# Optimization experiments

Hardware: AMD Instinct MI355X
Metric: run time of the kernel (lower is better)

The kernel has to match this reference:

```python
import jax, jax.numpy as jnp
import numpy as np

B, N, M, NS = 4, 32768, 1024, 32
RADIUS = 0.1
EPS = 1e-5
CHANS = [16, 32, 32, 64]


def setup_inputs() -> dict:
    key = jax.random.key(0)
    ks = jax.random.split(key, 8)
    d = {
        'theta': jax.random.uniform(ks[0], (B, N), jnp.float32, 0.0, float(np.pi)),
        'phi': jax.random.uniform(ks[1], (B, N), jnp.float32, 0.0, 2.0 * float(np.pi)),
        'features': jax.random.normal(ks[2], (B, CHANS[0], N), jnp.float32),
    }
    for i, (ci, co) in enumerate(zip(CHANS[:-1], CHANS[1:])):
        d[f'w{i}'] = jax.random.normal(jax.random.fold_in(ks[3], i), (co, ci), jnp.float32) * 0.1
        d[f'b{i}'] = jnp.zeros((co,), jnp.float32)
        d[f'g{i}'] = jnp.ones((co,), jnp.float32)
        d[f'be{i}'] = jnp.zeros((co,), jnp.float32)
    return d


def _group(theta, phi, features):
    # angular ball query + random neighbor sampling (deterministic key),
    # duplicates padded with the first valid neighbor (max-pool invariant,
    # matching the torch code's sampling-with-replacement semantics).
    k1, k2 = jax.random.split(jax.random.key(42))
    n = theta.shape[1]
    cent_idx = jax.random.permutation(k1, n)[:M]                 # shared across batch, like torch code
    ct = theta[:, cent_idx]                                      # (B, M)
    cp = phi[:, cent_idx]
    th_s, ph_s = jax.lax.stop_gradient(theta), jax.lax.stop_gradient(phi)
    ct_s, cp_s = jax.lax.stop_gradient(ct), jax.lax.stop_gradient(cp)
    dist = jnp.sqrt((th_s[:, None, :] - ct_s[:, :, None]) ** 2 +
                    (ph_s[:, None, :] - cp_s[:, :, None]) ** 2)  # (B, M, N)
    mask = dist <= RADIUS
    scores = jnp.where(mask, jax.random.uniform(k2, dist.shape, jnp.float32), jnp.inf)
    _, idx = jax.lax.top_k(-scores, NS)                          # NS random in-ball indices, (B, M, NS)
    valid = jnp.take_along_axis(mask, idx, axis=-1)
    idx = jnp.where(valid, idx, idx[..., :1])                    # centroid itself is always valid at slot 0
    gathered = jax.vmap(lambda f, i: f[:, i])(features, idx)     # (B, C, M, NS)
    grouped = jnp.transpose(gathered, (0, 1, 3, 2))              # (B, C, NS, M)
    return ct, cp, grouped


def _mlp_max(x, params):
    # 1x1 conv + BatchNorm (batch stats, training mode) + ReLU stack, then max over nsample
    for w, b, g, be in params:
        x = jnp.einsum('oc,bcsm->bosm', w, x) + b[None, :, None, None]
        mu = x.mean(axis=(0, 2, 3), keepdims=True)
        var = x.var(axis=(0, 2, 3), keepdims=True)
        x = (x - mu) * jax.lax.rsqrt(var + EPS) * g[None, :, None, None] + be[None, :, None, None]
        x = jax.nn.relu(x)
    return x.max(axis=2)                                         # (B, C_out, M)


def reference(theta, phi, features, w0, b0, g0, be0, w1, b1, g1, be1, w2, b2, g2, be2):
    params = [(w0, b0, g0, be0), (w1, b1, g1, be1), (w2, b2, g2, be2)]
    ct, cp, grouped = _group(theta, phi, features)
    new_feats = _mlp_max(grouped, params)
    return ct, cp, new_feats
```

## Files before the change

kernel.cpp:

```cpp
#include <hip/hip_runtime.h>
#include <stdint.h>

#define N_PTS 32768
#define M_CENT 1024
#define B_SZ 4
#define NS 32
#define NR 64
#define P_TOT (B_SZ * NS * M_CENT)

#define GT 29
#define GP 58
#define NCELL (GT * GP)
#define INVF (1.0f / 0.11f)
#define CAPW 320

__device__ __forceinline__ int cell_t(float t) {
  return min(GT - 1, (int)(t * INVF));
}
__device__ __forceinline__ int cell_p(float p) {
  return min(GP - 1, (int)(p * INVF));
}

struct Key2 { uint32_t a, b; };

__device__ __forceinline__ uint32_t rotl32(uint32_t v, uint32_t r) {
  return (v << r) | (v >> (32u - r));
}

__device__ __forceinline__ void tf2x32(uint32_t k0, uint32_t k1,
                                       uint32_t& x0, uint32_t& x1) {
  uint32_t ks0 = k0, ks1 = k1, ks2 = k0 ^ k1 ^ 0x1BD11BDAu;
  x0 += ks0; x1 += ks1;
#define TF_ROUND(r) { x0 += x1; x1 = rotl32(x1, r); x1 ^= x0; }
  TF_ROUND(13u) TF_ROUND(15u) TF_ROUND(26u) TF_ROUND(6u)
  x0 += ks1; x1 += ks2 + 1u;
  TF_ROUND(17u) TF_ROUND(29u) TF_ROUND(16u) TF_ROUND(24u)
  x0 += ks2; x1 += ks0 + 2u;
  TF_ROUND(13u) TF_ROUND(15u) TF_ROUND(26u) TF_ROUND(6u)
  x0 += ks0; x1 += ks1 + 3u;
  TF_ROUND(17u) TF_ROUND(29u) TF_ROUND(16u) TF_ROUND(24u)
  x0 += ks1; x1 += ks2 + 4u;
  TF_ROUND(13u) TF_ROUND(15u) TF_ROUND(26u) TF_ROUND(6u)
  x0 += ks2; x1 += ks0 + 5u;
#undef TF_ROUND
}

__device__ __forceinline__ Key2 tf_block(Key2 k, uint32_t hi, uint32_t lo) {
  uint32_t x0 = hi, x1 = lo;
  tf2x32(k.a, k.b, x0, x1);
  Key2 r; r.a = x0; r.b = x1; return r;
}

__global__ __launch_bounds__(256) void prep_kernel(const float* __restrict__ theta,
                                                   const float* __restrict__ phi,
                                                   uint32_t* __restrict__ bits1,
                                                   uint32_t* __restrict__ bits2,
                                                   int* __restrict__ hist1,
                                                   int* __restrict__ hist2,
                                                   int* __restrict__ cellcnt) {
  int j = blockIdx.x * 256 + threadIdx.x;
  int b = j >> 15;
  float t = theta[j], p = phi[j];
  atomicAdd(&cellcnt[b * NCELL + cell_t(t) * GP + cell_p(p)], 1);
  if (j < N_PTS) {
    Key2 root; root.a = 0u; root.b = 42u;
    Key2 k1   = tf_block(root, 0u, 0u);
    Key2 keyA = tf_block(k1, 0u, 0u);
    Key2 sub1 = tf_block(k1, 0u, 1u);
    Key2 sub2 = tf_block(keyA, 0u, 1u);
    Key2 r1 = tf_block(sub1, 0u, (uint32_t)j);
    Key2 r2 = tf_block(sub2, 0u, (uint32_t)j);
    uint32_t v1 = r1.a ^ r1.b, v2 = r2.a ^ r2.b;
    bits1[j] = v1; bits2[j] = v2;
    atomicAdd(&hist1[v1 >> 16], 1);
    atomicAdd(&hist2[v2 >> 16], 1);
  }
}

__global__ __launch_bounds__(256) void transpose_kernel(const float* __restrict__ feat,
                                                        float* __restrict__ featT) {
  __shared__ float lds[16][65];
  int b = blockIdx.y;
  int n0 = blockIdx.x * 64;
  int tid = threadIdx.x;
#pragma unroll
  for (int k = 0; k < 4; ++k) {
    int v = tid + k * 256;
    int c = v >> 6, no = v & 63;
    lds[c][no] = feat[((size_t)(b * 16 + c) << 15) + n0 + no];
  }
  __syncthreads();
#pragma unroll
  for (int k = 0; k < 4; ++k) {
    int v = tid + k * 256;
    int no = v >> 4, c = v & 15;
    featT[((size_t)(b << 15) + n0 + no) * 16 + c] = lds[c][no];
  }
}

__global__ __launch_bounds__(256) void scans_kernel(const int* __restrict__ hist1,
                                                    const int* __restrict__ hist2,
                                                    int* __restrict__ gbase1,
                                                    int* __restrict__ gbase2,
                                                    const int* __restrict__ cellcnt,
                                                    int* __restrict__ cellpre,
                                                    int* __restrict__ cellcur) {
  __shared__ int s[256];
  int t = threadIdx.x;
  if (blockIdx.x < 2) {
    const int* hist = blockIdx.x == 0 ? hist1 : hist2;
    int* gbase = blockIdx.x == 0 ? gbase1 : gbase2;
    int sum = 0;
    for (int i = 0; i < 256; ++i) sum += hist[t * 256 + i];
    s[t] = sum;
    __syncthreads();
    if (t == 0) {
      int run = 0;
      for (int i = 0; i < 256; ++i) { int v = s[i]; s[i] = run; run += v; }
    }
    __syncthreads();
    gbase[t] = s[t];
  } else {
    int b = blockIdx.x - 2;
    const int* cnt = cellcnt + b * NCELL;
    int i0 = t * 7, i1 = min(i0 + 7, NCELL);
    int sum = 0;
    for (int i = i0; i < i1; ++i) sum += cnt[i];
    s[t] = sum;
    __syncthreads();
    for (int off = 1; off < 256; off <<= 1) {
      int v = (t >= off) ? s[t - off] : 0;
      __syncthreads();
      s[t] += v;
      __syncthreads();
    }
    int run = (t == 0) ? 0 : s[t - 1];
    for (int i = i0; i < i1; ++i) {
      cellpre[b * NCELL + i] = run;
      cellcur[b * NCELL + i] = run;
      run += cnt[i];
    }
  }
}

__global__ __launch_bounds__(256) void bucket_scan_kernel(const int* __restrict__ hist1,
                                                          const int* __restrict__ hist2,
                                                          const int* __restrict__ gbase1,
                                                          const int* __restrict__ gbase2,
                                                          int* __restrict__ prefix1,
                                                          int* __restrict__ prefix2,
                                                          int* __restrict__ cursor1,
                                                          int* __restrict__ cursor2) {
  __shared__ int s[256];
  const int* hist = blockIdx.y == 0 ? hist1 : hist2;
  const int* gbase = blockIdx.y == 0 ? gbase1 : gbase2;
  int* prefix = blockIdx.y == 0 ? prefix1 : prefix2;
  int* cursor = blockIdx.y == 0 ? cursor1 : cursor2;
  int g = blockIdx.x, t = threadIdx.x;
  int idx = g * 256 + t;
  int orig = hist[idx];
  s[t] = orig;
  __syncthreads();
  for (int off = 1; off < 256; off <<= 1) {
    int v = (t >= off) ? s[t - off] : 0;
    __syncthreads();
    s[t] += v;
    __syncthreads();
  }
  int pref = gbase[g] + s[t] - orig;
  prefix[idx] = pref;
  cursor[idx] = pref;
}

__global__ __launch_bounds__(256) void scatter_kernel(const float* __restrict__ theta,
                                                      const float* __restrict__ phi,
                                                      int* __restrict__ cellcur,
                                                      float4* __restrict__ pts4,
                                                      const uint32_t* __restrict__ bits1,
                                                      const uint32_t* __restrict__ bits2,
                                                      int* __restrict__ cursor1,
                                                      int* __restrict__ cursor2,
                                                      int* __restrict__ sorted1,
                                                      int* __restrict__ sorted2) {
  int j = blockIdx.x * 256 + threadIdx.x;
  int b = j >> 15, n = j & (N_PTS - 1);
  float t = theta[j], p = phi[j];
  int cell = b * NCELL + cell_t(t) * GP + cell_p(p);
  int pos = atomicAdd(&cellcur[cell], 1);
  pts4[(b << 15) + pos] = make_float4(t, p, __int_as_float(n), 0.0f);
  if (j < N_PTS) {
    int p1 = atomicAdd(&cursor1[bits1[j] >> 16], 1);
    sorted1[p1] = j;
    int p2 = atomicAdd(&cursor2[bits2[j] >> 16], 1);
    sorted2[p2] = j;
  }
}

__device__ __forceinline__ int exact_rank(const uint32_t* __restrict__ bits,
                                          const int* __restrict__ prefix,
                                          const int* __restrict__ hist,
                                          const int* __restrict__ sorted, int j) {
  uint32_t my = bits[j];
  int b = (int)(my >> 16);
  int start = prefix[b];
  int cnt = hist[b];
  int r = start;
  for (int i = 0; i < cnt; ++i) {
    int m = sorted[start + i];
    uint32_t vb = bits[m];
    if (vb < my || (vb == my && m < j)) ++r;
  }
  return r;
}

__global__ __launch_bounds__(256) void rank_scatter1_kernel(
    const uint32_t* __restrict__ bits1, const uint32_t* __restrict__ bits2,
    const int* __restrict__ prefix1, const int* __restrict__ prefix2,
    const int* __restrict__ hist1, const int* __restrict__ hist2,
    const int* __restrict__ sorted1, const int* __restrict__ sorted2,
    int* __restrict__ xmid, int* __restrict__ rank2) {
  int j = blockIdx.x * 256 + threadIdx.x;
  int r1 = exact_rank(bits1, prefix1, hist1, sorted1, j);
  xmid[r1] = j;
  rank2[j] = exact_rank(bits2, prefix2, hist2, sorted2, j);
}

__global__ __launch_bounds__(256) void scatter2_kernel(const int* __restrict__ rank2,
                                                       const int* __restrict__ xmid,
                                                       int* __restrict__ xfin) {
  int p = blockIdx.x * 256 + threadIdx.x;
  xfin[rank2[p]] = xmid[p];
}

__global__ __launch_bounds__(256) void select_kernel(
    const float* __restrict__ theta, const float* __restrict__ phi,
    const int* __restrict__ cent,
    const int* __restrict__ cellpre, const int* __restrict__ cellcnt,
    const float4* __restrict__ pts4,
    int* __restrict__ idx_buf, float* __restrict__ out_ct, float* __restrict__ out_cp) {
  __shared__ float wsc[4][CAPW];
  __shared__ int wsn[4][CAPW];
  int tid = threadIdx.x;
  int w = tid >> 6, lane = tid & 63;
  int bm = blockIdx.x * 4 + w;
  int b = bm >> 10, m = bm & 1023;
  int ci = cent[m];
  float ctv = theta[(b << 15) + ci];
  float cpv = phi[(b << 15) + ci];
  if (lane == 0) { out_ct[bm] = ctv; out_cp[bm] = cpv; }

  Key2 root; root.a = 0u; root.b = 42u;
  Key2 k2 = tf_block(root, 0u, 1u);
  uint32_t flat_base = (uint32_t)bm << 15;

  int tc = cell_t(ctv), pc = cell_p(cpv);
  int t0 = max(0, tc - 1), t1 = min(GT - 1, tc + 1);
  int p0 = max(0, pc - 1), p1 = min(GP - 1, pc + 1);
  int nct = t1 - t0 + 1, ncp = p1 - p0 + 1, ncells = nct * ncp;

  int cst = 0, ccn = 0;
  if (lane < ncells) {
    int cell = b * NCELL + (t0 + lane / ncp) * GP + (p0 + lane % ncp);
    cst = cellpre[cell];
    ccn = cellcnt[cell];
  }
  int sc9[9], cc9[9];
#pragma unroll
  for (int k = 0; k < 9; ++k) {
    sc9[k] = __shfl(cst, k);
    cc9[k] = __shfl(ccn, k);
  }
  int T = 0;
#pragma unroll
  for (int k = 0; k < 9; ++k) T += cc9[k];

  const float4* bpts = pts4 + ((size_t)b << 15);
  int wcnt = 0;
  for (int base = 0; base < T; base += 64) {
    int i = base + lane;
    bool hit = false; float sc = 0.0f; int n = 0;
    if (i < T) {
      int gidx = 0, acc = 0;
#pragma unroll
      for (int k = 0; k < 9; ++k) {
        int lo = acc; acc += cc9[k];
        if (i >= lo && i < acc) gidx = sc9[k] + (i - lo);
      }
      float4 pt = bpts[gidx];
      float dx = __fsub_rn(pt.x, ctv);
      float dy = __fsub_rn(pt.y, cpv);
      float d = __fsqrt_rn(__fadd_rn(__fmul_rn(dx, dx), __fmul_rn(dy, dy)));
      if (d <= 0.1f) {
        hit = true; n = __float_as_int(pt.z);
        Key2 r = tf_block(k2, 0u, flat_base + (uint32_t)n);
        uint32_t bits = r.a ^ r.b;
        sc = __uint_as_float(0x3f800000u | (bits >> 9)) - 1.0f;
      }
    }
    unsigned long long mask = __ballot(hit);
    int pos = wcnt + __popcll(mask & ((1ull << lane) - 1ull));
    if (hit && pos < CAPW) { wsc[w][pos] = sc; wsn[w][pos] = n; }
    wcnt = min(wcnt + (int)__popcll(mask), CAPW);
  }

  int mysel;
  if (wcnt <= 64) {
    float s = (lane < wcnt) ? wsc[w][lane] : 3.0e38f;
    int n = (lane < wcnt) ? wsn[w][lane] : 0x7fffffff;
#pragma unroll
    for (int k = 2; k <= 64; k <<= 1) {
#pragma unroll
      for (int jj = k >> 1; jj > 0; jj >>= 1) {
        float os = __shfl_xor(s, jj);
        int on = __shfl_xor(n, jj);
        bool lower = (lane & jj) == 0;
        bool dir = (lane & k) == 0;
        bool mineFirst = (s < os) || (s == os && n < on);
        bool takeMine = ((lower == mineFirst) == dir);
        s = takeMine ? s : os;
        n = takeMine ? n : on;
      }
    }
    int n0 = __shfl(n, 0);
    mysel = (lane < wcnt) ? n : n0;
  } else {
    float ls = -1.0f; int ln = -1;
    int sel0 = -1; mysel = -1;
    for (int r = 0; r < NS; ++r) {
      float best = 3.0e38f; int bn = 0x7fffffff;
      for (int i = lane; i < wcnt; i += 64) {
        float s = wsc[w][i]; int n = wsn[w][i];
        bool after = (s > ls) || (s == ls && n > ln);
        bool better = (s < best) || (s == best && n < bn);
        if (after && better) { best = s; bn = n; }
      }
      for (int off = 32; off; off >>= 1) {
        float os = __shfl_xor(best, off);
        int on = __shfl_xor(bn, off);
        if (os < best || (os == best && on < bn)) { best = os; bn = on; }
      }
      int chosen;
      if (best < 3.0e38f) { ls = best; ln = bn; chosen = bn; }
      else chosen = sel0;
      if (r == 0) sel0 = chosen;
      if (lane == r) mysel = chosen;
    }
  }
  if (lane < NS) idx_buf[bm * NS + lane] = mysel;
}

__device__ __forceinline__ float bn_relu(float y, float mu, float r, float g, float be) {
  float t = __fsub_rn(y, mu);
  t = __fmul_rn(t, r);
  t = __fmul_rn(t, g);
  t = __fadd_rn(t, be);
  return fmaxf(t, 0.0f);
}

template <int CO>
__device__ __forceinline__ void accum_stats_pad(const float* __restrict__ Yp,
                                                double* __restrict__ S, int tid, int bid) {
  if (tid < CO) {
    double s1 = 0.0, s2 = 0.0;
#pragma unroll
    for (int s = 0; s < NS; ++s) {
      double v = (double)Yp[tid * 33 + s];
      s1 += v; s2 += v * v;
    }
    double* base = S + (size_t)(bid & (NR - 1)) * (2 * CO);
    atomicAdd(base + tid, s1);
    atomicAdd(base + CO + tid, s2);
  }
}

__global__ __launch_bounds__(256) void pass1_kernel(
    const float* __restrict__ feat, const float* __restrict__ featT,
    const int* __restrict__ idx_buf,
    const float* __restrict__ w0, const float* __restrict__ b0,
    float* __restrict__ stash, double* __restrict__ stats, int mode) {
  __shared__ int idxs[NS];
  __shared__ float X1[512];
  __shared__ float Yp[32 * 33];
  int bm = blockIdx.x, tid = threadIdx.x, b = bm >> 10;
  if (tid < NS) idxs[tid] = idx_buf[bm * NS + tid];
  __syncthreads();
  if (mode == 3) {
    if (tid < 128) {
      int s = tid >> 2, c4 = tid & 3;
      float4 f = *reinterpret_cast<const float4*>(
          &featT[((size_t)(b << 15) + idxs[s]) * 16 + c4 * 4]);
      X1[(c4 * 4 + 0) * 32 + s] = f.x;
      X1[(c4 * 4 + 1) * 32 + s] = f.y;
      X1[(c4 * 4 + 2) * 32 + s] = f.z;
      X1[(c4 * 4 + 3) * 32 + s] = f.w;
    }
  } else {
    for (int v = tid; v < 512; v += 256) {
      int c = v >> 5, s = v & 31;
      float val = feat[(size_t)(b * 16 + c) * N_PTS + idxs[s]];
      X1[v] = val;
      if (mode == 1) stash[(size_t)bm * 512 + v] = val;
    }
  }
  __syncthreads();
  for (int v = tid; v < 1024; v += 256) {
    int o = v >> 5, s = v & 31;
    float acc = b0[o];
#pragma unroll
    for (int c = 0; c < 16; ++c) acc = fmaf(w0[o * 16 + c], X1[c * 32 + s], acc);
    Yp[o * 33 + s] = acc;
    if (mode >= 2) stash[(size_t)bm * 1024 + v] = acc;
  }
  __syncthreads();
  accum_stats_pad<32>(Yp, stats, tid, bm);
}

__global__ __launch_bounds__(256) void pass2s_kernel(
    const float* __restrict__ Y1g,
    const float* __restrict__ mur1, const float* __restrict__ g0, const float* __restrict__ be0,
    const float* __restrict__ w1, const float* __restrict__ b1,
    double* __restrict__ stats) {
  __shared__ float X2[1024];
  __shared__ float Yp[32 * 33];
  int bm = blockIdx.x, tid = threadIdx.x;
  for (int v = tid; v < 1024; v += 256) {
    int o = v >> 5;
    X2[v] = bn_relu(Y1g[(size_t)bm * 1024 + v], mur1[o], mur1[32 + o], g0[o], be0[o]);
  }
  __syncthreads();
  for (int v = tid; v < 1024; v += 256) {
    int o = v >> 5, s = v & 31;
    float acc = b1[o];
#pragma unroll
    for (int c = 0; c < 32; ++c) acc = fmaf(w1[o * 32 + c], X2[c * 32 + s], acc);
    Yp[o * 33 + s] = acc;
  }
  __syncthreads();
  accum_stats_pad<32>(Yp, stats, tid, bm);
}

__global__ __launch_bounds__(256) void pass3s_kernel(
    const float* __restrict__ Y1g,
    const float* __restrict__ mur1, const float* __restrict__ g0, const float* __restrict__ be0,
    const float* __restrict__ w1, const float* __restrict__ b1,
    const float* __restrict__ mur2, const float* __restrict__ g1, const float* __restrict__ be1,
    const float* __restrict__ w2, const float* __restrict__ b2,
    float* __restrict__ mm3, double* __restrict__ stats) {
  __shared__ float X2[1024];
  __shared__ float X3[1024];
  __shared__ float Yp[64 * 33];
  int bm = blockIdx.x, tid = threadIdx.x;
  for (int v = tid; v < 1024; v += 256) {
    int o = v >> 5;
    X2[v] = bn_relu(Y1g[(size_t)bm * 1024 + v], mur1[o], mur1[32 + o], g0[o], be0[o]);
  }
  __syncthreads();
  for (int v = tid; v < 1024; v += 256) {
    int o = v >> 5, s = v & 31;
    float acc = b1[o];
#pragma unroll
    for (int c = 0; c < 32; ++c) acc = fmaf(w1[o * 32 + c], X2[c * 32 + s], acc);
    X3[v] = bn_relu(acc, mur2[o], mur2[32 + o], g1[o], be1[o]);
  }
  __syncthreads();
  for (int v = tid; v < 2048; v += 256) {
    int o = v >> 5, s = v & 31;
    float acc = b2[o];
#pragma unroll
    for (int c = 0; c < 32; ++c) acc = fmaf(w2[o * 32 + c], X3[c * 32 + s], acc);
    Yp[o * 33 + s] = acc;
  }
  __syncthreads();
  if (tid < 64) {
    double s1 = 0.0, s2 = 0.0;
    float mx = -3.0e38f, mn = 3.0e38f;
#pragma unroll
    for (int s = 0; s < NS; ++s) {
      float y = Yp[tid * 33 + s];
      double v = (double)y;
      s1 += v; s2 += v * v;
      mx = fmaxf(mx, y); mn = fminf(mn, y);
    }
    double* base = stats + (size_t)(bm & (NR - 1)) * 128;
    atomicAdd(base + tid, s1);
    atomicAdd(base + 64 + tid, s2);
    mm3[bm * 128 + tid * 2] = mx;
    mm3[bm * 128 + tid * 2 + 1] = mn;
  }
}

__global__ __launch_bounds__(256) void final_small_kernel(
    const float* __restrict__ mm3,
    const float* __restrict__ mur3, const float* __restrict__ g2, const float* __restrict__ be2,
    float* __restrict__ out_ft) {
  int j = blockIdx.x * 256 + threadIdx.x;
  int b = j >> 16, o = (j >> 10) & 63, m = j & 1023;
  int bm = b * 1024 + m;
  float g = g2[o];
  float y = (g >= 0.0f) ? mm3[bm * 128 + o * 2] : mm3[bm * 128 + o * 2 + 1];
  out_ft[j] = bn_relu(y, mur3[o], mur3[64 + o], g, be2[o]);
}

__device__ __forceinline__ void load_x1(int big, const float* __restrict__ X1g,
                                        const float* __restrict__ feat,
                                        const int* __restrict__ idx_buf,
                                        int bm, int b, int tid,
                                        int* idxs, float* X1) {
  if (!big) {
    if (tid < NS) idxs[tid] = idx_buf[bm * NS + tid];
  }
  __syncthreads();
  if (big) {
    for (int v = tid; v < 512; v += 256) X1[v] = X1g[(size_t)bm * 512 + v];
  } else {
    for (int v = tid; v < 512; v += 256) {
      int c = v >> 5, s = v & 31;
      X1[v] = feat[(size_t)(b * 16 + c) * N_PTS + idxs[s]];
    }
  }
}

__global__ __launch_bounds__(256) void pass2_rec_kernel(
    const float* __restrict__ X1g, const float* __restrict__ feat,
    const int* __restrict__ idx_buf,
    const float* __restrict__ w0, const float* __restrict__ b0,
    const float* __restrict__ mur1, const float* __restrict__ g0, const float* __restrict__ be0,
    const float* __restrict__ w1, const float* __restrict__ b1,
    double* __restrict__ stats, int big) {
  __shared__ int idxs[NS];
  __shared__ float X1[512];
  __shared__ float X2[1024];
  __shared__ float Yp[32 * 33];
  int bm = blockIdx.x, tid = threadIdx.x, b = bm >> 10;
  load_x1(big, X1g, feat, idx_buf, bm, b, tid, idxs, X1);
  __syncthreads();
  for (int v = tid; v < 1024; v += 256) {
    int o = v >> 5, s = v & 31;
    float acc = b0[o];
#pragma unroll
    for (int c = 0; c < 16; ++c) acc = fmaf(w0[o * 16 + c], X1[c * 32 + s], acc);
    X2[v] = bn_relu(acc, mur1[o], mur1[32 + o], g0[o], be0[o]);
  }
  __syncthreads();
  for (int v = tid; v < 1024; v += 256) {
    int o = v >> 5, s = v & 31;
    float acc = b1[o];
#pragma unroll
    for (int c = 0; c < 32; ++c) acc = fmaf(w1[o * 32 + c], X2[c * 32 + s], acc);
    Yp[o * 33 + s] = acc;
  }
  __syncthreads();
  accum_stats_pad<32>(Yp, stats, tid, bm);
}

__global__ __launch_bounds__(256) void pass3_rec_kernel(
    const float* __restrict__ X1g, const float* __restrict__ feat,
    const int* __restrict__ idx_buf,
    const float* __restrict__ w0, const float* __restrict__ b0,
    const float* __restrict__ mur1, const float* __restrict__ g0, const float* __restrict__ be0,
    const float* __restrict__ w1, const float* __restrict__ b1,
    const float* __restrict__ mur2, const float* __restrict__ g1, const float* __restrict__ be1,
    const float* __restrict__ w2, const float* __restrict__ b2,
    float* __restrict__ mm3, double* __restrict__ stats, int big) {
  __shared__ int idxs[NS];
  __shared__ float X1[512];
  __shared__ float X2[1024];
  __shared__ float X3[1024];
  __shared__ float Yp[64 * 33];
  int bm = blockIdx.x, tid = threadIdx.x, b = bm >> 10;
  load_x1(big, X1g, feat, idx_buf, bm, b, tid, idxs, X1);
  __syncthreads();
  for (int v = tid; v < 1024; v += 256) {
    int o = v >> 5, s = v & 31;
    float acc = b0[o];
#pragma unroll
    for (int c = 0; c < 16; ++c) acc = fmaf(w0[o * 16 + c], X1[c * 32 + s], acc);
    X2[v] = bn_relu(acc, mur1[o], mur1[32 + o], g0[o], be0[o]);
  }
  __syncthreads();
  for (int v = tid; v < 1024; v += 256) {
    int o = v >> 5, s = v & 31;
    float acc = b1[o];
#pragma unroll
    for (int c = 0; c < 32; ++c) acc = fmaf(w1[o * 32 + c], X2[c * 32 + s], acc);
    X3[v] = bn_relu(acc, mur2[o], mur2[32 + o], g1[o], be1[o]);
  }
  __syncthreads();
  for (int v = tid; v < 2048; v += 256) {
    int o = v >> 5, s = v & 31;
    float acc = b2[o];
#pragma unroll
    for (int c = 0; c < 32; ++c) acc = fmaf(w2[o * 32 + c], X3[c * 32 + s], acc);
    Yp[o * 33 + s] = acc;
  }
  __syncthreads();
  if (tid < 64) {
    double s1 = 0.0, s2 = 0.0;
    float mx = -3.0e38f, mn = 3.0e38f;
#pragma unroll
    for (int s = 0; s < NS; ++s) {
      float y = Yp[tid * 33 + s];
      double v = (double)y;
      s1 += v; s2 += v * v;
      mx = fmaxf(mx, y); mn = fminf(mn, y);
    }
    double* base = stats + (size_t)(bm & (NR - 1)) * 128;
    atomicAdd(base + tid, s1);
    atomicAdd(base + 64 + tid, s2);
    mm3[bm * 128 + tid * 2] = mx;
    mm3[bm * 128 + tid * 2 + 1] = mn;
  }
}

template <int CO>
__global__ void fixup_mur_kernel(const double* __restrict__ S, float* __restrict__ mur) {
  int o = threadIdx.x;
  if (o >= CO) return;
  double s1 = 0.0, s2 = 0.0;
  for (int r = 0; r < NR; ++r) {
    s1 += S[r * 2 * CO + o];
    s2 += S[r * 2 * CO + CO + o];
  }
  const double P = (double)P_TOT;
  double mu = s1 / P;
  double var = s2 / P - mu * mu;
  mur[o] = (float)mu;
  mur[CO + o] = (float)(1.0 / sqrt(var + 1e-5));
}

extern "C" void kernel_launch(void* const* d_in, const int* in_sizes, int n_in,
                              void* d_out, int out_size, void* d_ws, size_t ws_size,
                              hipStream_t stream) {
  (void)in_sizes; (void)n_in; (void)out_size;
  const float* theta = (const float*)d_in[0];
  const float* phi   = (const float*)d_in[1];
  const float* feat  = (const float*)d_in[2];
  const float* w0 = (const float*)d_in[3];
  const float* b0 = (const float*)d_in[4];
  const float* g0 = (const float*)d_in[5];
  const float* be0 = (const float*)d_in[6];
  const float* w1 = (const float*)d_in[7];
  const float* b1 = (const float*)d_in[8];
  const float* g1 = (const float*)d_in[9];
  const float* be1 = (const float*)d_in[10];
  const float* w2 = (const float*)d_in[11];
  const float* b2 = (const float*)d_in[12];
  const float* g2 = (const float*)d_in[13];
  const float* be2 = (const float*)d_in[14];

  float* out = (float*)d_out;
  float* out_ct = out;
  float* out_cp = out + B_SZ * M_CENT;
  float* out_ft = out + 2 * B_SZ * M_CENT;

  char* ws = (char*)d_ws;
  uint32_t* bits1 = (uint32_t*)(ws + 0);
  uint32_t* bits2 = (uint32_t*)(ws + 131072);
  int* rank2 = (int*)(ws + 262144);
  int* xmid  = (int*)(ws + 393216);
  int* xfin  = (int*)(ws + 524288);
  int* idx_buf = (int*)(ws + 655360);
  int* hist1   = (int*)(ws + 1179648);
  int* hist2   = (int*)(ws + 1441792);
  int* cellcnt = (int*)(ws + 1703936);
  double* stats1 = (double*)(ws + 1736704);
  double* stats2 = (double*)(ws + 1769472);
  double* stats3 = (double*)(ws + 1802240);
  int* prefix1 = (int*)(ws + 1867776);
  int* prefix2 = (int*)(ws + 2129920);
  int* cursor1 = (int*)(ws + 2392064);
  int* cursor2 = (int*)(ws + 2654208);
  int* sorted1 = (int*)(ws + 2916352);
  int* sorted2 = (int*)(ws + 3047424);
  int* gbase1  = (int*)(ws + 3178496);
  int* gbase2  = (int*)(ws + 3179520);
  int* cellpre = (int*)(ws + 3180544);
  int* cellcur = (int*)(ws + 3213312);
  float4* pts4 = (float4*)(ws + 3246080);
  float* mur1 = (float*)(ws + 5343232);
  float* mur2 = (float*)(ws + 5343488);
  float* mur3 = (float*)(ws + 5343744);
  float* mm3  = (float*)(ws + 5344768);
  float* stash = (float*)(ws + 7441920);
  float* featT = (float*)(ws + 7441920 + 16777216);
  size_t NEED_FULL = (size_t)7441920 + 16777216;
  size_t NEED_T    = NEED_FULL + 8388608;
  size_t NEED_BIG  = (size_t)7441920 + 8388608;
  int mode = (ws_size >= NEED_T) ? 3
           : (ws_size >= NEED_FULL) ? 2
           : (ws_size >= NEED_BIG) ? 1 : 0;

  hipMemsetAsync(ws + 1179648, 0, 688128, stream);

  prep_kernel<<<512, 256, 0, stream>>>(theta, phi, bits1, bits2, hist1, hist2, cellcnt);
  if (mode == 3)
    transpose_kernel<<<dim3(512, 4), 256, 0, stream>>>(feat, featT);
  scans_kernel<<<6, 256, 0, stream>>>(hist1, hist2, gbase1, gbase2,
                                      cellcnt, cellpre, cellcur);
  bucket_scan_kernel<<<dim3(256, 2), 256, 0, stream>>>(hist1, hist2, gbase1, gbase2,
                                                       prefix1, prefix2, cursor1, cursor2);
  scatter_kernel<<<512, 256, 0, stream>>>(theta, phi, cellcur, pts4,
                                          bits1, bits2, cursor1, cursor2,
                                          sorted1, sorted2);
  rank_scatter1_kernel<<<128, 256, 0, stream>>>(bits1, bits2, prefix1, prefix2,
                                                hist1, hist2, sorted1, sorted2,
                                                xmid, rank2);
  scatter2_kernel<<<128, 256, 0, stream>>>(rank2, xmid, xfin);

  select_kernel<<<1024, 256, 0, stream>>>(theta, phi, xfin, cellpre, cellcnt,
                                          pts4, idx_buf, out_ct, out_cp);

  pass1_kernel<<<4096, 256, 0, stream>>>(feat, featT, idx_buf, w0, b0, stash, stats1, mode);
  fixup_mur_kernel<32><<<1, 64, 0, stream>>>(stats1, mur1);
  if (mode >= 2) {
    pass2s_kernel<<<4096, 256, 0, stream>>>(stash, mur1, g0, be0, w1, b1, stats2);
    fixup_mur_kernel<32><<<1, 64, 0, stream>>>(stats2, mur2);
    pass3s_kernel<<<4096, 256, 0, stream>>>(stash, mur1, g0, be0, w1, b1,
                                            mur2, g1, be1, w2, b2, mm3, stats3);
  } else {
    pass2_rec_kernel<<<4096, 256, 0, stream>>>(stash, feat, idx_buf, w0, b0, mur1, g0, be0,
                                               w1, b1, stats2, mode);
    fixup_mur_kernel<32><<<1, 64, 0, stream>>>(stats2, mur2);
    pass3_rec_kernel<<<4096, 256, 0, stream>>>(stash, feat, idx_buf, w0, b0, mur1, g0, be0,
                                               w1, b1, mur2, g1, be1, w2, b2, mm3, stats3, mode);
  }
  fixup_mur_kernel<64><<<1, 64, 0, stream>>>(stats3, mur3);
  final_small_kernel<<<1024, 256, 0, stream>>>(mm3, mur3, g2, be2, out_ft);
}
```

Measured before the change: 277.0 us.

## Map one thread per grouped point in MLP passes with wave-shuffle stat reduction

The three MLP/BatchNorm kernels are rewritten so each thread owns one (centroid, sample) point and keeps its channel vector in registers, instead of one block per centroid staging through shared memory. Per-channel sums and max/min are reduced with wavefront shuffles and fp32 partials before the fp64 atomics. The grid shrinks from 4096 to 512 blocks. The low-workspace recompute fallbacks are removed and the workspace is now assumed large enough for the stash. The change adds register pressure and many more atomics per block, and the fp32 partial sums lose some precision.

Result: slower. 288.4 us (+4.1%).

```diff
diff --git a/kernel.cpp b/kernel.cpp
--- a/kernel.cpp
+++ b/kernel.cpp
@@ -357,135 +357,139 @@
   return fmaxf(t, 0.0f);
 }
 
-template <int CO>
-__device__ __forceinline__ void accum_stats_pad(const float* __restrict__ Yp,
-                                                double* __restrict__ S, int tid, int bid) {
-  if (tid < CO) {
-    double s1 = 0.0, s2 = 0.0;
-#pragma unroll
-    for (int s = 0; s < NS; ++s) {
-      double v = (double)Yp[tid * 33 + s];
-      s1 += v; s2 += v * v;
-    }
-    double* base = S + (size_t)(bid & (NR - 1)) * (2 * CO);
-    atomicAdd(base + tid, s1);
-    atomicAdd(base + CO + tid, s2);
-  }
-}
-
-__global__ __launch_bounds__(256) void pass1_kernel(
+__global__ __launch_bounds__(256) void l1_kernel(
     const float* __restrict__ feat, const float* __restrict__ featT,
     const int* __restrict__ idx_buf,
     const float* __restrict__ w0, const float* __restrict__ b0,
-    float* __restrict__ stash, double* __restrict__ stats, int mode) {
-  __shared__ int idxs[NS];
-  __shared__ float X1[512];
-  __shared__ float Yp[32 * 33];
-  int bm = blockIdx.x, tid = threadIdx.x, b = bm >> 10;
-  if (tid < NS) idxs[tid] = idx_buf[bm * NS + tid];
-  __syncthreads();
-  if (mode == 3) {
-    if (tid < 128) {
-      int s = tid >> 2, c4 = tid & 3;
-      float4 f = *reinterpret_cast<const float4*>(
-          &featT[((size_t)(b << 15) + idxs[s]) * 16 + c4 * 4]);
-      X1[(c4 * 4 + 0) * 32 + s] = f.x;
-      X1[(c4 * 4 + 1) * 32 + s] = f.y;
-      X1[(c4 * 4 + 2) * 32 + s] = f.z;
-      X1[(c4 * 4 + 3) * 32 + s] = f.w;
+    float* __restrict__ Y1g, double* __restrict__ stats, int useT) {
+  int j = blockIdx.x * 256 + threadIdx.x;
+  int bm = j >> 5, s = j & 31, b = bm >> 10;
+  int lane = threadIdx.x & 63;
+  int idx = idx_buf[j];
+  float x[16];
+  if (useT) {
+    const float4* src = reinterpret_cast<const float4*>(
+        featT + (((size_t)b << 15) + (size_t)idx) * 16);
+#pragma unroll
+    for (int q = 0; q < 4; ++q) {
+      float4 f = src[q];
+      x[q * 4 + 0] = f.x; x[q * 4 + 1] = f.y;
+      x[q * 4 + 2] = f.z; x[q * 4 + 3] = f.w;
     }
   } else {
-    for (int v = tid; v < 512; v += 256) {
-      int c = v >> 5, s = v & 31;
-      float val = feat[(size_t)(b * 16 + c) * N_PTS + idxs[s]];
-      X1[v] = val;
-      if (mode == 1) stash[(size_t)bm * 512 + v] = val;
-    }
-  }
-  __syncthreads();
-  for (int v = tid; v < 1024; v += 256) {
-    int o = v >> 5, s = v & 31;
+#pragma unroll
+    for (int c = 0; c < 16; ++c)
+      x[c] = feat[((size_t)(b * 16 + c) << 15) + idx];
+  }
+  float y[32];
+#pragma unroll
+  for (int o = 0; o < 32; ++o) {
     float acc = b0[o];
 #pragma unroll
-    for (int c = 0; c < 16; ++c) acc = fmaf(w0[o * 16 + c], X1[c * 32 + s], acc);
-    Yp[o * 33 + s] = acc;
-    if (mode >= 2) stash[(size_t)bm * 1024 + v] = acc;
-  }
-  __syncthreads();
-  accum_stats_pad<32>(Yp, stats, tid, bm);
-}
-
-__global__ __launch_bounds__(256) void pass2s_kernel(
+    for (int c = 0; c < 16; ++c) acc = fmaf(w0[o * 16 + c], x[c], acc);
+    y[o] = acc;
+    Y1g[(size_t)bm * 1024 + o * 32 + s] = acc;
+  }
+  int rep = (j >> 6) & (NR - 1);
+  double* base = stats + (size_t)rep * 64;
+#pragma unroll
+  for (int o = 0; o < 32; ++o) {
+    float s1 = y[o], s2 = y[o] * y[o];
+#pragma unroll
+    for (int off = 32; off; off >>= 1) {
+      s1 += __shfl_xor(s1, off);
+      s2 += __shfl_xor(s2, off);
+    }
+    if (lane == 0) {
+      atomicAdd(base + o, (double)s1);
+      atomicAdd(base + 32 + o, (double)s2);
+    }
+  }
+}
+
+__global__ __launch_bounds__(256) void l2_kernel(
     const float* __restrict__ Y1g,
     const float* __restrict__ mur1, const float* __restrict__ g0, const float* __restrict__ be0,
     const float* __restrict__ w1, const float* __restrict__ b1,
     double* __restrict__ stats) {
-  __shared__ float X2[1024];
-  __shared__ float Yp[32 * 33];
-  int bm = blockIdx.x, tid = threadIdx.x;
-  for (int v = tid; v < 1024; v += 256) {
-    int o = v >> 5;
-    X2[v] = bn_relu(Y1g[(size_t)bm * 1024 + v], mur1[o], mur1[32 + o], g0[o], be0[o]);
-  }
-  __syncthreads();
-  for (int v = tid; v < 1024; v += 256) {
-    int o = v >> 5, s = v & 31;
+  int j = blockIdx.x * 256 + threadIdx.x;
+  int bm = j >> 5, s = j & 31;
+  int lane = threadIdx.x & 63;
+  float x2[32];
+#pragma unroll
+  for (int c = 0; c < 32; ++c)
+    x2[c] = bn_relu(Y1g[(size_t)bm * 1024 + c * 32 + s],
+                    mur1[c], mur1[32 + c], g0[c], be0[c]);
+  int rep = (j >> 6) & (NR - 1);
+  double* base = stats + (size_t)rep * 64;
+#pragma unroll
+  for (int o = 0; o < 32; ++o) {
     float acc = b1[o];
 #pragma unroll
-    for (int c = 0; c < 32; ++c) acc = fmaf(w1[o * 32 + c], X2[c * 32 + s], acc);
-    Yp[o * 33 + s] = acc;
-  }
-  __syncthreads();
-  accum_stats_pad<32>(Yp, stats, tid, bm);
-}
-
-__global__ __launch_bounds__(256) void pass3s_kernel(
+    for (int c = 0; c < 32; ++c) acc = fmaf(w1[o * 32 + c], x2[c], acc);
+    float s1 = acc, s2 = acc * acc;
+#pragma unroll
+    for (int off = 32; off; off >>= 1) {
+      s1 += __shfl_xor(s1, off);
+      s2 += __shfl_xor(s2, off);
+    }
+    if (lane == 0) {
+      atomicAdd(base + o, (double)s1);
+      atomicAdd(base + 32 + o, (double)s2);
+    }
+  }
+}
+
+__global__ __launch_bounds__(256) void l3_kernel(
     const float* __restrict__ Y1g,
     const float* __restrict__ mur1, const float* __restrict__ g0, const float* __restrict__ be0,
     const float* __restrict__ w1, const float* __restrict__ b1,
     const float* __restrict__ mur2, const float* __restrict__ g1, const float* __restrict__ be1,
     const float* __restrict__ w2, const float* __restrict__ b2,
     float* __restrict__ mm3, double* __restrict__ stats) {
-  __shared__ float X2[1024];
-  __shared__ float X3[1024];
-  __shared__ float Yp[64 * 33];
-  int bm = blockIdx.x, tid = threadIdx.x;
-  for (int v = tid; v < 1024; v += 256) {
-    int o = v >> 5;
-    X2[v] = bn_relu(Y1g[(size_t)bm * 1024 + v], mur1[o], mur1[32 + o], g0[o], be0[o]);
-  }
-  __syncthreads();
-  for (int v = tid; v < 1024; v += 256) {
-    int o = v >> 5, s = v & 31;
+  int j = blockIdx.x * 256 + threadIdx.x;
+  int bm = j >> 5, s = j & 31;
+  int lane = threadIdx.x & 63;
+  float x2[32];
+#pragma unroll
+  for (int c = 0; c < 32; ++c)
+    x2[c] = bn_relu(Y1g[(size_t)bm * 1024 + c * 32 + s],
+                    mur1[c], mur1[32 + c], g0[c], be0[c]);
+  float x3[32];
+#pragma unroll
+  for (int o = 0; o < 32; ++o) {
     float acc = b1[o];
 #pragma unroll
-    for (int c = 0; c < 32; ++c) acc = fmaf(w1[o * 32 + c], X2[c * 32 + s], acc);
-    X3[v] = bn_relu(acc, mur2[o], mur2[32 + o], g1[o], be1[o]);
-  }
-  __syncthreads();
-  for (int v = tid; v < 2048; v += 256) {
-    int o = v >> 5, s = v & 31;
+    for (int c = 0; c < 32; ++c) acc = fmaf(w1[o * 32 + c], x2[c], acc);
+    x3[o] = bn_relu(acc, mur2[o], mur2[32 + o], g1[o], be1[o]);
+  }
+  int rep = (j >> 6) & (NR - 1);
+  double* base = stats + (size_t)rep * 128;
+#pragma unroll
+  for (int o = 0; o < 64; ++o) {
     float acc = b2[o];
 #pragma unroll
-    for (int c = 0; c < 32; ++c) acc = fmaf(w2[o * 32 + c], X3[c * 32 + s], acc);
-    Yp[o * 33 + s] = acc;
-  }
-  __syncthreads();
-  if (tid < 64) {
-    double s1 = 0.0, s2 = 0.0;
-    float mx = -3.0e38f, mn = 3.0e38f;
-#pragma unroll
-    for (int s = 0; s < NS; ++s) {
-      float y = Yp[tid * 33 + s];
-      double v = (double)y;
-      s1 += v; s2 += v * v;
-      mx = fmaxf(mx, y); mn = fminf(mn, y);
-    }
-    double* base = stats + (size_t)(bm & (NR - 1)) * 128;
-    atomicAdd(base + tid, s1);
-    atomicAdd(base + 64 + tid, s2);
-    mm3[bm * 128 + tid * 2] = mx;
-    mm3[bm * 128 + tid * 2 + 1] = mn;
+    for (int c = 0; c < 32; ++c) acc = fmaf(w2[o * 32 + c], x3[c], acc);
+    float s1 = acc, s2 = acc * acc;
+#pragma unroll
+    for (int off = 32; off; off >>= 1) {
+      s1 += __shfl_xor(s1, off);
+      s2 += __shfl_xor(s2, off);
+    }
+    if (lane == 0) {
+      atomicAdd(base + o, (double)s1);
+      atomicAdd(base + 64 + o, (double)s2);
+    }
+    float mx = acc, mn = acc;
+#pragma unroll
+    for (int off = 16; off; off >>= 1) {
+      mx = fmaxf(mx, __shfl_xor(mx, off));
+      mn = fminf(mn, __shfl_xor(mn, off));
+    }
+    if (s == 0) {
+      mm3[bm * 128 + o * 2] = mx;
+      mm3[bm * 128 + o * 2 + 1] = mn;
+    }
   }
 }
 
@@ -499,117 +503,6 @@
   float g = g2[o];
   float y = (g >= 0.0f) ? mm3[bm * 128 + o * 2] : mm3[bm * 128 + o * 2 + 1];
   out_ft[j] = bn_relu(y, mur3[o], mur3[64 + o], g, be2[o]);
-}
-
-__device__ __forceinline__ void load_x1(int big, const float* __restrict__ X1g,
-                                        const float* __restrict__ feat,
-                                        const int* __restrict__ idx_buf,
-                                        int bm, int b, int tid,
-                                        int* idxs, float* X1) {
-  if (!big) {
-    if (tid < NS) idxs[tid] = idx_buf[bm * NS + tid];
-  }
-  __syncthreads();
-  if (big) {
-    for (int v = tid; v < 512; v += 256) X1[v] = X1g[(size_t)bm * 512 + v];
-  } else {
-    for (int v = tid; v < 512; v += 256) {
-      int c = v >> 5, s = v & 31;
-      X1[v] = feat[(size_t)(b * 16 + c) * N_PTS + idxs[s]];
-    }
-  }
-}
-
-__global__ __launch_bounds__(256) void pass2_rec_kernel(
-    const float* __restrict__ X1g, const float* __restrict__ feat,
-    const int* __restrict__ idx_buf,
-    const float* __restrict__ w0, const float* __restrict__ b0,
-    const float* __restrict__ mur1, const float* __restrict__ g0, const float* __restrict__ be0,
-    const float* __restrict__ w1, const float* __restrict__ b1,
-    double* __restrict__ stats, int big) {
-  __shared__ int idxs[NS];
-  __shared__ float X1[512];
-  __shared__ float X2[1024];
-  __shared__ float Yp[32 * 33];
-  int bm = blockIdx.x, tid = threadIdx.x, b = bm >> 10;
-  load_x1(big, X1g, feat, idx_buf, bm, b, tid, idxs, X1);
-  __syncthreads();
-  for (int v = tid; v < 1024; v += 256) {
-    int o = v >> 5, s = v & 31;
-    float acc = b0[o];
-#pragma unroll
-    for (int c = 0; c < 16; ++c) acc = fmaf(w0[o * 16 + c], X1[c * 32 + s], acc);
-    X2[v] = bn_relu(acc, mur1[o], mur1[32 + o], g0[o], be0[o]);
-  }
-  __syncthreads();
-  for (int v = tid; v < 1024; v += 256) {
-    int o = v >> 5, s = v & 31;
-    float acc = b1[o];
-#pragma unroll
-    for (int c = 0; c < 32; ++c) acc = fmaf(w1[o * 32 + c], X2[c * 32 + s], acc);
-    Yp[o * 33 + s] = acc;
-  }
-  __syncthreads();
-  accum_stats_pad<32>(Yp, stats, tid, bm);
-}
-
-__global__ __launch_bounds__(256) void pass3_rec_kernel(
-    const float* __restrict__ X1g, const float* __restrict__ feat,
-    const int* __restrict__ idx_buf,
-    const float* __restrict__ w0, const float* __restrict__ b0,
-    const float* __restrict__ mur1, const float* __restrict__ g0, const float* __restrict__ be0,
-    const float* __restrict__ w1, const float* __restrict__ b1,
-    const float* __restrict__ mur2, const float* __restrict__ g1, const float* __restrict__ be1,
-    const float* __restrict__ w2, const float* __restrict__ b2,
-    float* __restrict__ mm3, double* __restrict__ stats, int big) {
-  __shared__ int idxs[NS];
-  __shared__ float X1[512];
-  __shared__ float X2[1024];
-  __shared__ float X3[1024];
-  __shared__ float Yp[64 * 33];
-  int bm = blockIdx.x, tid = threadIdx.x, b = bm >> 10;
-  load_x1(big, X1g, feat, idx_buf, bm, b, tid, idxs, X1);
-  __syncthreads();
-  for (int v = tid; v < 1024; v += 256) {
-    int o = v >> 5, s = v & 31;
-    float acc = b0[o];
-#pragma unroll
-    for (int c = 0; c < 16; ++c) acc = fmaf(w0[o * 16 + c], X1[c * 32 + s], acc);
-    X2[v] = bn_relu(acc, mur1[o], mur1[32 + o], g0[o], be0[o]);
-  }
-  __syncthreads();
-  for (int v = tid; v < 1024; v += 256) {
-    int o = v >> 5, s = v & 31;
-    float acc = b1[o];
-#pragma unroll
-    for (int c = 0; c < 32; ++c) acc = fmaf(w1[o * 32 + c], X2[c * 32 + s], acc);
-    X3[v] = bn_relu(acc, mur2[o], mur2[32 + o], g1[o], be1[o]);
-  }
-  __syncthreads();
-  for (int v = tid; v < 2048; v += 256) {
-    int o = v >> 5, s = v & 31;
-    float acc = b2[o];
-#pragma unroll
-    for (int c = 0; c < 32; ++c) acc = fmaf(w2[o * 32 + c], X3[c * 32 + s], acc);
-    Yp[o * 33 + s] = acc;
-  }
-  __syncthreads();
-  if (tid < 64) {
-    double s1 = 0.0, s2 = 0.0;
-    float mx = -3.0e38f, mn = 3.0e38f;
-#pragma unroll
-    for (int s = 0; s < NS; ++s) {
-      float y = Yp[tid * 33 + s];
-      double v = (double)y;
-      s1 += v; s2 += v * v;
-      mx = fmaxf(mx, y); mn = fminf(mn, y);
-    }
-    double* base = stats + (size_t)(bm & (NR - 1)) * 128;
-    atomicAdd(base + tid, s1);
-    atomicAdd(base + 64 + tid, s2);
-    mm3[bm * 128 + tid * 2] = mx;
-    mm3[bm * 128 + tid * 2 + 1] = mn;
-  }
 }
 
 template <int CO>
@@ -681,19 +574,15 @@
   float* mur2 = (float*)(ws + 5343488);
   float* mur3 = (float*)(ws + 5343744);
   float* mm3  = (float*)(ws + 5344768);
-  float* stash = (float*)(ws + 7441920);
+  float* Y1g  = (float*)(ws + 7441920);
   float* featT = (float*)(ws + 7441920 + 16777216);
-  size_t NEED_FULL = (size_t)7441920 + 16777216;
-  size_t NEED_T    = NEED_FULL + 8388608;
-  size_t NEED_BIG  = (size_t)7441920 + 8388608;
-  int mode = (ws_size >= NEED_T) ? 3
-           : (ws_size >= NEED_FULL) ? 2
-           : (ws_size >= NEED_BIG) ? 1 : 0;
+  size_t NEED_T = (size_t)7441920 + 16777216 + 8388608;
+  int useT = (ws_size >= NEED_T) ? 1 : 0;
 
   hipMemsetAsync(ws + 1179648, 0, 688128, stream);
 
   prep_kernel<<<512, 256, 0, stream>>>(theta, phi, bits1, bits2, hist1, hist2, cellcnt);
-  if (mode == 3)
+  if (useT)
     transpose_kernel<<<dim3(512, 4), 256, 0, stream>>>(feat, featT);
   scans_kernel<<<6, 256, 0, stream>>>(hist1, hist2, gbase1, gbase2,
                                       cellcnt, cellpre, cellcur);
@@ -710,20 +599,12 @@
   select_kernel<<<1024, 256, 0, stream>>>(theta, phi, xfin, cellpre, cellcnt,
                                           pts4, idx_buf, out_ct, out_cp);
 
-  pass1_kernel<<<4096, 256, 0, stream>>>(feat, featT, idx_buf, w0, b0, stash, stats1, mode);
+  l1_kernel<<<512, 256, 0, stream>>>(feat, featT, idx_buf, w0, b0, Y1g, stats1, useT);
   fixup_mur_kernel<32><<<1, 64, 0, stream>>>(stats1, mur1);
-  if (mode >= 2) {
-    pass2s_kernel<<<4096, 256, 0, stream>>>(stash, mur1, g0, be0, w1, b1, stats2);
-    fixup_mur_kernel<32><<<1, 64, 0, stream>>>(stats2, mur2);
-    pass3s_kernel<<<4096, 256, 0, stream>>>(stash, mur1, g0, be0, w1, b1,
-                                            mur2, g1, be1, w2, b2, mm3, stats3);
-  } else {
-    pass2_rec_kernel<<<4096, 256, 0, stream>>>(stash, feat, idx_buf, w0, b0, mur1, g0, be0,
-                                               w1, b1, stats2, mode);
-    fixup_mur_kernel<32><<<1, 64, 0, stream>>>(stats2, mur2);
-    pass3_rec_kernel<<<4096, 256, 0, stream>>>(stash, feat, idx_buf, w0, b0, mur1, g0, be0,
-                                               w1, b1, mur2, g1, be1, w2, b2, mm3, stats3, mode);
-  }
+  l2_kernel<<<512, 256, 0, stream>>>(Y1g, mur1, g0, be0, w1, b1, stats2);
+  fixup_mur_kernel<32><<<1, 64, 0, stream>>>(stats2, mur2);
+  l3_kernel<<<512, 256, 0, stream>>>(Y1g, mur1, g0, be0, w1, b1,
+                                     mur2, g1, be1, w2, b2, mm3, stats3);
   fixup_mur_kernel<64><<<1, 64, 0, stream>>>(stats3, mur3);
   final_small_kernel<<<1024, 256, 0, stream>>>(mm3, mur3, g2, be2, out_ft);
 }
```
